# Kernel tuning notes

Hardware: AMD Instinct MI355X
Metric: run time of the kernel (lower is better)

Reference implementation:

```python
import jax, jax.numpy as jnp
import numpy as np

B, S, D, H = 2, 2048, 768, 12
DH = D // H  # 64


def setup_inputs() -> dict:
    key = jax.random.key(0)
    ks = jax.random.split(key, 8)
    std = 1.0 / np.sqrt(D)
    return {
        "q": jax.random.normal(ks[0], (B, S, D), dtype=jnp.float32),
        "k": jax.random.normal(ks[1], (B, S, D), dtype=jnp.float32),
        "v": jax.random.normal(ks[2], (B, S, D), dtype=jnp.float32),
        "Wq": jax.random.normal(ks[3], (D, D), dtype=jnp.float32) * std,
        "bq": jnp.zeros((D,), dtype=jnp.float32),
        "Wk": jax.random.normal(ks[4], (D, D), dtype=jnp.float32) * std,
        "bk": jnp.zeros((D,), dtype=jnp.float32),
        "Wv": jax.random.normal(ks[5], (D, D), dtype=jnp.float32) * std,
        "bv": jnp.zeros((D,), dtype=jnp.float32),
        "Wo": jax.random.normal(ks[6], (D, D), dtype=jnp.float32) * std,
        "bo": jnp.zeros((D,), dtype=jnp.float32),
    }


def reference(q, k, v, Wq, bq, Wk, bk, Wv, bv, Wo, bo):
    b, s, d = q.shape
    # linear projections then split heads: [b, s, d] -> [b, h, s, dh]
    def split(x):
        return x.reshape(b, s, H, DH).transpose(0, 2, 1, 3)

    qh = split(q @ Wq + bq)
    kh = split(k @ Wk + bk)
    vh = split(v @ Wv + bv)

    scale = 1.0 / jnp.sqrt(jnp.asarray(DH, dtype=q.dtype))
    # full [b, h, s, s] score matrix (faithful to the original unfused op)
    scores = jnp.einsum("bhqd,bhkd->bhqk", qh, kh) * scale
    # look-ahead mask: 1 above the diagonal, added as mask * -1e9
    look_ahead = jnp.triu(jnp.ones((s, s), dtype=scores.dtype), k=1)
    scores = scores + look_ahead * (-1e9)

    attn = jax.nn.softmax(scores, axis=-1)  # dropout is identity at inference
    ctx = jnp.einsum("bhqk,bhkd->bhqd", attn, vh)
    ctx = ctx.transpose(0, 2, 1, 3).reshape(b, s, d)
    return ctx @ Wo + bo
```

## Files before the change

kernel.cpp:

```cpp
#include <hip/hip_runtime.h>
#include <hip/hip_bf16.h>
#include <stdint.h>

#define Bz 2
#define Sz 2048
#define Dz 768
#define Hz 12
#define DHz 64
#define Mz (Bz*Sz)
#define NQT16 128

typedef __attribute__((ext_vector_type(4))) float f32x4;
typedef __attribute__((ext_vector_type(8))) short bf16x8;
typedef unsigned short u16;
typedef __attribute__((ext_vector_type(8))) unsigned short u16x8;

__device__ __forceinline__ u16 f2bf(float f) {
  union { float f; uint32_t u; } c; c.f = f;
  uint32_t u = c.u;
  return (u16)((u + 0x7fffu + ((u >> 16) & 1u)) >> 16);
}

__device__ __forceinline__ uint32_t packbf(float lo, float hi) {
  return (uint32_t)f2bf(lo) | ((uint32_t)f2bf(hi) << 16);
}

#define GLL16(gsrc, ldst) \
  __builtin_amdgcn_global_load_lds((const __attribute__((address_space(1))) void*)(gsrc), \
                                   (__attribute__((address_space(3))) void*)(ldst), 16, 0, 0)

__device__ __forceinline__ f32x4 mfma16(bf16x8 a, bf16x8 b, f32x4 c) {
  return __builtin_amdgcn_mfma_f32_16x16x32_bf16(a, b, c, 0, 0, 0);
}

#define CVTB 1536
__global__ __launch_bounds__(256) void prep_kernel(
    const float* __restrict__ qa, const float* __restrict__ ka, const float* __restrict__ va,
    u16* __restrict__ qo, u16* __restrict__ ko, u16* __restrict__ vo,
    const float* __restrict__ W0, const float* __restrict__ W1,
    const float* __restrict__ W2, const float* __restrict__ W3,
    u16* __restrict__ T0, u16* __restrict__ T1,
    u16* __restrict__ T2, u16* __restrict__ T3)
{
  __shared__ float tile[32][33];
  int bid = blockIdx.x;
  if (bid < 3 * CVTB) {
    int z = bid / CVTB;
    int i = (bid % CVTB) * 256 + threadIdx.x;
    const float* src = (z == 0) ? qa : (z == 1) ? ka : va;
    u16* dst = (z == 0) ? qo : (z == 1) ? ko : vo;
    const float4* s4 = (const float4*)src;
    float4 a = s4[(size_t)i * 2];
    float4 b = s4[(size_t)i * 2 + 1];
    u16x8 o;
    o[0] = f2bf(a.x); o[1] = f2bf(a.y); o[2] = f2bf(a.z); o[3] = f2bf(a.w);
    o[4] = f2bf(b.x); o[5] = f2bf(b.y); o[6] = f2bf(b.z); o[7] = f2bf(b.w);
    *(u16x8*)(dst + (size_t)i * 8) = o;
  } else {
    int w = bid - 3 * CVTB;
    int z = w / 576;
    int rem = w - z * 576;
    int by = rem / 24, bxi = rem - by * 24;
    const float* W = (z == 0) ? W0 : (z == 1) ? W1 : (z == 2) ? W2 : W3;
    u16* Wt = (z == 0) ? T0 : (z == 1) ? T1 : (z == 2) ? T2 : T3;
    int bx = bxi * 32, byy = by * 32;
    int tx = threadIdx.x & 31, ty = threadIdx.x >> 5;
#pragma unroll
    for (int i = 0; i < 32; i += 8)
      tile[ty + i][tx] = W[(size_t)(byy + ty + i) * Dz + bx + tx];
    __syncthreads();
#pragma unroll
    for (int i = 0; i < 32; i += 8)
      Wt[(size_t)(bx + ty + i) * Dz + byy + tx] = f2bf(tile[tx][ty + i]);
  }
}

__device__ __forceinline__ void gemm_core(
    const u16* __restrict__ A, const u16* __restrict__ Wt,
    const float* __restrict__ bias, void* __restrict__ out, int mode, float oscale,
    u16 (*As)[128 * 32], u16 (*Bs)[128 * 32])
{
  const int tid = threadIdx.x;
  const int wid = tid >> 6, lane = tid & 63;
  const int wm = wid >> 1, wn = wid & 1;
  const int m0 = blockIdx.x * 128, n0 = blockIdx.y * 128;
  const int fq = lane >> 4, fr = lane & 15;

  int aoff[2];
#pragma unroll
  for (int c = 0; c < 2; ++c) {
    int off  = (wid * 2 + c) * 1024 + lane * 16;
    int row  = off >> 6;
    int colb = (off & 63) ^ (((row >> 1) & 3) << 4);
    aoff[c]  = row * Dz + (colb >> 1);
  }

  int raddr[4], rbaddr[4];
#pragma unroll
  for (int f = 0; f < 4; ++f) {
    int rowA = wm * 64 + f * 16 + fr;
    raddr[f]  = rowA * 64 + ((fq * 16) ^ (((rowA >> 1) & 3) << 4));
    int rowB = wn * 64 + f * 16 + fr;
    rbaddr[f] = rowB * 64 + ((fq * 16) ^ (((rowB >> 1) & 3) << 4));
  }

  f32x4 acc[4][4];
  const f32x4 zero = {0.f, 0.f, 0.f, 0.f};
#pragma unroll
  for (int i = 0; i < 4; ++i)
#pragma unroll
    for (int j = 0; j < 4; ++j) acc[i][j] = zero;

  const u16* Abase = A + (size_t)m0 * Dz;
  const u16* Bbase = Wt + (size_t)n0 * Dz;

  const int NKT = Dz / 32;
#pragma unroll
  for (int c = 0; c < 2; ++c) {
    GLL16(Abase + aoff[c], (char*)As[0] + (wid * 2 + c) * 1024);
    GLL16(Bbase + aoff[c], (char*)Bs[0] + (wid * 2 + c) * 1024);
  }
  int cur = 0;

  for (int kt = 0; kt < NKT; ++kt) {
    int nx = cur + 1; if (nx == 3) nx = 0;
    if (kt + 1 < NKT) {
      int ke = (kt + 1) * 32;
#pragma unroll
      for (int c = 0; c < 2; ++c) {
        GLL16(Abase + ke + aoff[c], (char*)As[nx] + (wid * 2 + c) * 1024);
        GLL16(Bbase + ke + aoff[c], (char*)Bs[nx] + (wid * 2 + c) * 1024);
      }
      asm volatile("s_waitcnt vmcnt(4)" ::: "memory");
    } else {
      asm volatile("s_waitcnt vmcnt(0)" ::: "memory");
    }
    __builtin_amdgcn_s_barrier();
    __builtin_amdgcn_sched_barrier(0);

    bf16x8 af[4], bf[4];
#pragma unroll
    for (int f = 0; f < 4; ++f) {
      af[f] = *(const bf16x8*)((const char*)As[cur] + raddr[f]);
      bf[f] = *(const bf16x8*)((const char*)Bs[cur] + rbaddr[f]);
    }
    __builtin_amdgcn_s_setprio(1);
#pragma unroll
    for (int i = 0; i < 4; ++i)
#pragma unroll
      for (int j = 0; j < 4; ++j)
        acc[i][j] = mfma16(af[i], bf[j], acc[i][j]);
    __builtin_amdgcn_s_setprio(0);
    cur = nx;
  }

  {
    u16* O = (u16*)out;
#pragma unroll
    for (int i = 0; i < 4; ++i) {
      int grow = m0 + wm * 64 + i * 16 + fq * 4;
#pragma unroll
      for (int j = 0; j < 4; ++j) {
        int gcol = n0 + wn * 64 + j * 16 + fr;
        float bv = bias[gcol];
        int h = gcol >> 6, dh = gcol & 63;
#pragma unroll
        for (int r = 0; r < 4; ++r) {
          int t = grow + r;
          int b = t >> 11, s = t & 2047;
          int bh = b * Hz + h;
          u16 val = f2bf((acc[i][j][r] + bv) * oscale);
          size_t idx;
          if (mode == 0) {
            idx = ((((size_t)bh * 128 + (s >> 4)) * 2 + (dh >> 5)) * 64
                   + ((dh >> 3) & 3) * 16 + (s & 15)) * 8 + (dh & 7);
          } else if (mode == 3) {
            idx = (((((size_t)bh * 32 + (s >> 6)) * 4 + ((s >> 4) & 3)) * 2 + (dh >> 5)) * 64
                   + ((dh >> 3) & 3) * 16 + (s & 15)) * 8 + (dh & 7);
          } else {
            int K  = s & 63;
            int pk = ((K & 15) << 2) | (K >> 4);
            idx = (((((size_t)bh * 32 + (s >> 6)) * 4 + (dh >> 4)) * 2 + (pk >> 5)) * 64
                   + ((pk >> 3) & 3) * 16 + (dh & 15)) * 8 + (pk & 7);
          }
          O[idx] = val;
        }
      }
    }
  }
}

__device__ __forceinline__ void gemm_out_core64(
    const u16* __restrict__ A, const u16* __restrict__ Wt,
    const float* __restrict__ bias, float* __restrict__ O,
    u16 (*As)[64 * 32], u16 (*Bs)[128 * 32])
{
  const int tid = threadIdx.x;
  const int wid = tid >> 6, lane = tid & 63;
  const int wm = wid >> 1, wn = wid & 1;
  const int m0 = blockIdx.x * 64, n0 = blockIdx.y * 128;
  const int fq = lane >> 4, fr = lane & 15;

  int aoff;
  {
    int off  = tid * 16;
    int row  = off >> 6;
    int colb = (off & 63) ^ (((row >> 1) & 3) << 4);
    aoff = row * Dz + (colb >> 1);
  }
  int boff[2];
#pragma unroll
  for (int c = 0; c < 2; ++c) {
    int off  = tid * 16 + c * 4096;
    int row  = off >> 6;
    int colb = (off & 63) ^ (((row >> 1) & 3) << 4);
    boff[c] = row * Dz + (colb >> 1);
  }

  int raddr[2], rbaddr[4];
#pragma unroll
  for (int f = 0; f < 2; ++f) {
    int rowA = wm * 32 + f * 16 + fr;
    raddr[f] = rowA * 64 + ((fq * 16) ^ (((rowA >> 1) & 3) << 4));
  }
#pragma unroll
  for (int f = 0; f < 4; ++f) {
    int rowB = wn * 64 + f * 16 + fr;
    rbaddr[f] = rowB * 64 + ((fq * 16) ^ (((rowB >> 1) & 3) << 4));
  }

  f32x4 acc[2][4];
  const f32x4 zero = {0.f, 0.f, 0.f, 0.f};
#pragma unroll
  for (int i = 0; i < 2; ++i)
#pragma unroll
    for (int j = 0; j < 4; ++j) acc[i][j] = zero;

  const u16* Abase = A + (size_t)m0 * Dz;
  const u16* Bbase = Wt + (size_t)n0 * Dz;

  const int NKT = Dz / 32;
  GLL16(Abase + aoff, (char*)As[0] + tid * 16);
#pragma unroll
  for (int c = 0; c < 2; ++c)
    GLL16(Bbase + boff[c], (char*)Bs[0] + tid * 16 + c * 4096);
  int cur = 0;

  for (int kt = 0; kt < NKT; ++kt) {
    int nx = cur + 1; if (nx == 3) nx = 0;
    if (kt + 1 < NKT) {
      int ke = (kt + 1) * 32;
      GLL16(Abase + ke + aoff, (char*)As[nx] + tid * 16);
#pragma unroll
      for (int c = 0; c < 2; ++c)
        GLL16(Bbase + ke + boff[c], (char*)Bs[nx] + tid * 16 + c * 4096);
      asm volatile("s_waitcnt vmcnt(3)" ::: "memory");
    } else {
      asm volatile("s_waitcnt vmcnt(0)" ::: "memory");
    }
    __builtin_amdgcn_s_barrier();
    __builtin_amdgcn_sched_barrier(0);

    bf16x8 af[2], bf[4];
#pragma unroll
    for (int f = 0; f < 2; ++f)
      af[f] = *(const bf16x8*)((const char*)As[cur] + raddr[f]);
#pragma unroll
    for (int f = 0; f < 4; ++f)
      bf[f] = *(const bf16x8*)((const char*)Bs[cur] + rbaddr[f]);
    __builtin_amdgcn_s_setprio(1);
#pragma unroll
    for (int i = 0; i < 2; ++i)
#pragma unroll
      for (int j = 0; j < 4; ++j)
        acc[i][j] = mfma16(af[i], bf[j], acc[i][j]);
    __builtin_amdgcn_s_setprio(0);
    cur = nx;
  }

#pragma unroll
  for (int i = 0; i < 2; ++i) {
    int grow = m0 + wm * 32 + i * 16 + fq * 4;
#pragma unroll
    for (int j = 0; j < 4; ++j) {
      int gcol = n0 + wn * 64 + j * 16 + fr;
      float bv = bias[gcol];
#pragma unroll
      for (int r = 0; r < 4; ++r)
        O[(size_t)(grow + r) * Dz + gcol] = acc[i][j][r] + bv;
    }
  }
}

#define QSCALE 0.1803368801111404f

__global__ __launch_bounds__(256, 3) void gemm_qkv(
    const u16* __restrict__ qb, const u16* __restrict__ kb, const u16* __restrict__ vb,
    const u16* __restrict__ Wqt, const u16* __restrict__ Wkt, const u16* __restrict__ Wvt,
    const float* __restrict__ bq, const float* __restrict__ bk, const float* __restrict__ bv,
    u16* __restrict__ Qf, u16* __restrict__ Kf, u16* __restrict__ Vf)
{
  __shared__ u16 As[3][128 * 32];
  __shared__ u16 Bs[3][128 * 32];
  const u16* A; const u16* W; const float* bias; u16* out; int mode; float osc;
  if (blockIdx.z == 0)      { A = qb; W = Wqt; bias = bq; out = Qf; mode = 0; osc = QSCALE; }
  else if (blockIdx.z == 1) { A = kb; W = Wkt; bias = bk; out = Kf; mode = 3; osc = 1.f; }
  else                      { A = vb; W = Wvt; bias = bv; out = Vf; mode = 1; osc = 1.f; }
  gemm_core(A, W, bias, out, mode, osc, As, Bs);
}

__global__ __launch_bounds__(256, 4) void gemm_out_k(
    const u16* __restrict__ ctx, const u16* __restrict__ Wot,
    const float* __restrict__ bo, float* __restrict__ out)
{
  __shared__ u16 As[3][64 * 32];
  __shared__ u16 Bs[3][128 * 32];
  gemm_out_core64(ctx, Wot, bo, out, As, Bs);
}

__global__ __launch_bounds__(128, 2) void attn_kernel(
    const u16* __restrict__ Qf, const u16* __restrict__ Kf,
    const u16* __restrict__ Vf, u16* __restrict__ ctx)
{
  __shared__ u16 Ps[2][16 * 64];
  __shared__ float o1buf[64 * 16];
  __shared__ float ml1[2][16];
  const int tid = threadIdx.x, wid = tid >> 6, lane = tid & 63;
  const int fq = lane >> 4, fr = lane & 15;
  const int bh = blockIdx.x;
  const int qt = (NQT16 - 1) - blockIdx.y;
  const int b = bh / Hz, h = bh % Hz;
  const int qbase = qt * 16;
  const int nkt = (qbase + 79) >> 6;

  const bf16x8* Qf8 = (const bf16x8*)Qf + (size_t)bh * 128 * 2 * 64;
  const bf16x8* Kf8 = (const bf16x8*)Kf + (size_t)bh * 32 * 8 * 64;
  const bf16x8* Vf8 = (const bf16x8*)Vf + (size_t)bh * 32 * 8 * 64;

  bf16x8 aq[2];
#pragma unroll
  for (int kk = 0; kk < 2; ++kk)
    aq[kk] = Qf8[((size_t)qt * 2 + kk) * 64 + lane];

  const f32x4 zero = {0.f, 0.f, 0.f, 0.f};
  f32x4 o[4];
#pragma unroll
  for (int i = 0; i < 4; ++i) o[i] = zero;
  float m_r[4], l_r[4];
#pragma unroll
  for (int r = 0; r < 4; ++r) { m_r[r] = -1e30f; l_r[r] = 0.f; }

  char* Pw = (char*)Ps[wid];

  if (wid < nkt) {
    bf16x8 kfr[4][2], vfr[4][2];
#pragma unroll
    for (int j = 0; j < 4; ++j)
#pragma unroll
      for (int kk = 0; kk < 2; ++kk)
        kfr[j][kk] = Kf8[((size_t)wid * 8 + j * 2 + kk) * 64 + lane];

    for (int kt = wid; kt < nkt; kt += 2) {
#pragma unroll
      for (int fo = 0; fo < 4; ++fo)
#pragma unroll
        for (int kk = 0; kk < 2; ++kk)
          vfr[fo][kk] = Vf8[((size_t)kt * 8 + fo * 2 + kk) * 64 + lane];

      f32x4 s[4];
#pragma unroll
      for (int j = 0; j < 4; ++j) s[j] = zero;
      __builtin_amdgcn_s_setprio(1);
#pragma unroll
      for (int j = 0; j < 4; ++j)
#pragma unroll
        for (int kk = 0; kk < 2; ++kk)
          s[j] = mfma16(aq[kk], kfr[j][kk], s[j]);
      __builtin_amdgcn_s_setprio(0);

      if (kt + 2 < nkt) {
#pragma unroll
        for (int j = 0; j < 4; ++j)
#pragma unroll
          for (int kk = 0; kk < 2; ++kk)
            kfr[j][kk] = Kf8[((size_t)(kt + 2) * 8 + j * 2 + kk) * 64 + lane];
      }

      if (kt == nkt - 1) {
#pragma unroll
        for (int j = 0; j < 4; ++j) {
          int keyg = kt * 64 + j * 16 + fr;
#pragma unroll
          for (int r = 0; r < 4; ++r)
            if (keyg > qbase + fq * 4 + r) s[j][r] = -1e30f;
        }
      }

      float mt[4];
#pragma unroll
      for (int r = 0; r < 4; ++r) mt[r] = s[0][r];
#pragma unroll
      for (int j = 1; j < 4; ++j)
#pragma unroll
        for (int r = 0; r < 4; ++r) mt[r] = fmaxf(mt[r], s[j][r]);

      int nd = 0;
#pragma unroll
      for (int r = 0; r < 4; ++r) nd |= (mt[r] > m_r[r] + 8.f) ? 1 : 0;
      if (__any(nd)) {
#pragma unroll
        for (int msk = 1; msk < 16; msk <<= 1)
#pragma unroll
          for (int r = 0; r < 4; ++r) mt[r] = fmaxf(mt[r], __shfl_xor(mt[r], msk));
#pragma unroll
        for (int r = 0; r < 4; ++r) {
          float mn = fmaxf(m_r[r], mt[r]);
          float alpha = __builtin_amdgcn_exp2f(m_r[r] - mn);
          m_r[r] = mn;
          l_r[r] *= alpha;
#pragma unroll
          for (int i = 0; i < 4; ++i) o[i][r] *= alpha;
        }
      }

#pragma unroll
      for (int r = 0; r < 4; ++r) {
        float e0 = __builtin_amdgcn_exp2f(s[0][r] - m_r[r]);
        float e1 = __builtin_amdgcn_exp2f(s[1][r] - m_r[r]);
        float e2 = __builtin_amdgcn_exp2f(s[2][r] - m_r[r]);
        float e3 = __builtin_amdgcn_exp2f(s[3][r] - m_r[r]);
        l_r[r] += (e0 + e1) + (e2 + e3);
        uint2 w;
        w.x = packbf(e0, e1);
        w.y = packbf(e2, e3);
        int qr = fq * 4 + r;
        *(uint2*)(Pw + qr * 128 + ((fr * 8) ^ ((qr & 7) << 4))) = w;
      }

      __builtin_amdgcn_s_setprio(1);
#pragma unroll
      for (int kk = 0; kk < 2; ++kk) {
        int cbP = (kk * 64 + fq * 16) ^ ((fr & 7) << 4);
        bf16x8 pa = *(const bf16x8*)(Pw + fr * 128 + cbP);
#pragma unroll
        for (int fo = 0; fo < 4; ++fo)
          o[fo] = mfma16(pa, vfr[fo][kk], o[fo]);
      }
      __builtin_amdgcn_s_setprio(0);
    }
  }

#pragma unroll
  for (int msk = 1; msk < 16; msk <<= 1)
#pragma unroll
    for (int r = 0; r < 4; ++r) l_r[r] += __shfl_xor(l_r[r], msk);

  if (wid == 1) {
#pragma unroll
    for (int fo = 0; fo < 4; ++fo)
#pragma unroll
      for (int r = 0; r < 4; ++r)
        o1buf[lane * 16 + fo * 4 + r] = o[fo][r];
    if (fr == 0) {
#pragma unroll
      for (int r = 0; r < 4; ++r) {
        ml1[0][fq * 4 + r] = m_r[r];
        ml1[1][fq * 4 + r] = l_r[r];
      }
    }
  }
  __syncthreads();

  if (wid == 0) {
    float a0[4], a1[4], li[4];
#pragma unroll
    for (int r = 0; r < 4; ++r) {
      float m1 = ml1[0][fq * 4 + r];
      float l1 = ml1[1][fq * 4 + r];
      float mm = fmaxf(m_r[r], m1);
      a0[r] = __builtin_amdgcn_exp2f(m_r[r] - mm);
      a1[r] = __builtin_amdgcn_exp2f(m1 - mm);
      li[r] = 1.0f / (l_r[r] * a0[r] + l1 * a1[r]);
    }
#pragma unroll
    for (int fo = 0; fo < 4; ++fo) {
      int dh = fo * 16 + fr;
#pragma unroll
      for (int r = 0; r < 4; ++r) {
        float o1 = o1buf[lane * 16 + fo * 4 + r];
        float val = (o[fo][r] * a0[r] + o1 * a1[r]) * li[r];
        int qg = qbase + fq * 4 + r;
        ctx[((size_t)b * Sz + qg) * Dz + h * DHz + dh] = f2bf(val);
      }
    }
  }
}

extern "C" void kernel_launch(void* const* d_in, const int* in_sizes, int n_in,
                              void* d_out, int out_size, void* d_ws, size_t ws_size,
                              hipStream_t stream) {
  const float* q  = (const float*)d_in[0];
  const float* k  = (const float*)d_in[1];
  const float* v  = (const float*)d_in[2];
  const float* Wq = (const float*)d_in[3];
  const float* bq = (const float*)d_in[4];
  const float* Wk = (const float*)d_in[5];
  const float* bk = (const float*)d_in[6];
  const float* Wv = (const float*)d_in[7];
  const float* bv = (const float*)d_in[8];
  const float* Wo = (const float*)d_in[9];
  const float* bo = (const float*)d_in[10];
  float* out = (float*)d_out;

  char* ws = (char*)d_ws;
  size_t off = 0;
  auto alloc = [&](size_t bytes) {
    void* p = ws + off;
    off += (bytes + 255) & ~(size_t)255;
    return p;
  };
  u16* qb  = (u16*)alloc((size_t)Mz * Dz * 2);
  u16* kb  = (u16*)alloc((size_t)Mz * Dz * 2);
  u16* vb  = (u16*)alloc((size_t)Mz * Dz * 2);
  u16* Wqt = (u16*)alloc((size_t)Dz * Dz * 2);
  u16* Wkt = (u16*)alloc((size_t)Dz * Dz * 2);
  u16* Wvt = (u16*)alloc((size_t)Dz * Dz * 2);
  u16* Wot = (u16*)alloc((size_t)Dz * Dz * 2);
  u16* Qf  = (u16*)alloc((size_t)Bz * Hz * Sz * DHz * 2);
  u16* Kf  = (u16*)alloc((size_t)Bz * Hz * Sz * DHz * 2);
  u16* Vf  = (u16*)alloc((size_t)Bz * Hz * Sz * DHz * 2);
  u16* ctx = (u16*)alloc((size_t)Mz * Dz * 2);

  prep_kernel<<<3 * CVTB + 4 * 576, 256, 0, stream>>>(
      q, k, v, qb, kb, vb, Wq, Wk, Wv, Wo, Wqt, Wkt, Wvt, Wot);

  gemm_qkv<<<dim3(Mz / 128, Dz / 128, 3), 256, 0, stream>>>(
      qb, kb, vb, Wqt, Wkt, Wvt, bq, bk, bv, Qf, Kf, Vf);

  attn_kernel<<<dim3(Bz * Hz, NQT16), 128, 0, stream>>>(Qf, Kf, Vf, ctx);

  gemm_out_k<<<dim3(Mz / 64, Dz / 128), 256, 0, stream>>>(ctx, Wot, bo, out);
}
```

Measured before the change: 89.63 us.

## Split attention KV loop across four waves per query tile

Each attention block now runs four waves instead of two. The waves stride over key tiles by four, and the partial max, sum and output of waves 1–3 are merged by wave 0 through shared memory. This shortens the serial KV loop per query tile, which matters most for long causal rows, and raises the number of waves in flight. In exchange, shared memory and merge work grow, and for short query tiles some waves sit idle.

```diff
diff --git a/kernel.cpp b/kernel.cpp
--- a/kernel.cpp
+++ b/kernel.cpp
@@ -318,13 +318,13 @@
   gemm_out_core64(ctx, Wot, bo, out, As, Bs);
 }
 
-__global__ __launch_bounds__(128, 2) void attn_kernel(
+__global__ __launch_bounds__(256, 4) void attn_kernel(
     const u16* __restrict__ Qf, const u16* __restrict__ Kf,
     const u16* __restrict__ Vf, u16* __restrict__ ctx)
 {
-  __shared__ u16 Ps[2][16 * 64];
-  __shared__ float o1buf[64 * 16];
-  __shared__ float ml1[2][16];
+  __shared__ u16 Ps[4][16 * 64];
+  __shared__ float obuf[3][64 * 16];
+  __shared__ float mlb[3][2][16];
   const int tid = threadIdx.x, wid = tid >> 6, lane = tid & 63;
   const int fq = lane >> 4, fr = lane & 15;
   const int bh = blockIdx.x;
@@ -360,7 +360,7 @@
       for (int kk = 0; kk < 2; ++kk)
         kfr[j][kk] = Kf8[((size_t)wid * 8 + j * 2 + kk) * 64 + lane];
 
-    for (int kt = wid; kt < nkt; kt += 2) {
+    for (int kt = wid; kt < nkt; kt += 4) {
 #pragma unroll
       for (int fo = 0; fo < 4; ++fo)
 #pragma unroll
@@ -378,12 +378,12 @@
           s[j] = mfma16(aq[kk], kfr[j][kk], s[j]);
       __builtin_amdgcn_s_setprio(0);
 
-      if (kt + 2 < nkt) {
+      if (kt + 4 < nkt) {
 #pragma unroll
         for (int j = 0; j < 4; ++j)
 #pragma unroll
           for (int kk = 0; kk < 2; ++kk)
-            kfr[j][kk] = Kf8[((size_t)(kt + 2) * 8 + j * 2 + kk) * 64 + lane];
+            kfr[j][kk] = Kf8[((size_t)(kt + 4) * 8 + j * 2 + kk) * 64 + lane];
       }
 
       if (kt == nkt - 1) {
@@ -455,40 +455,54 @@
 #pragma unroll
     for (int r = 0; r < 4; ++r) l_r[r] += __shfl_xor(l_r[r], msk);
 
-  if (wid == 1) {
+  if (wid > 0) {
 #pragma unroll
     for (int fo = 0; fo < 4; ++fo)
 #pragma unroll
       for (int r = 0; r < 4; ++r)
-        o1buf[lane * 16 + fo * 4 + r] = o[fo][r];
+        obuf[wid - 1][lane * 16 + fo * 4 + r] = o[fo][r];
     if (fr == 0) {
 #pragma unroll
       for (int r = 0; r < 4; ++r) {
-        ml1[0][fq * 4 + r] = m_r[r];
-        ml1[1][fq * 4 + r] = l_r[r];
+        mlb[wid - 1][0][fq * 4 + r] = m_r[r];
+        mlb[wid - 1][1][fq * 4 + r] = l_r[r];
       }
     }
   }
   __syncthreads();
 
   if (wid == 0) {
-    float a0[4], a1[4], li[4];
+    float mm[4], lsum[4], a0[4];
 #pragma unroll
     for (int r = 0; r < 4; ++r) {
-      float m1 = ml1[0][fq * 4 + r];
-      float l1 = ml1[1][fq * 4 + r];
-      float mm = fmaxf(m_r[r], m1);
-      a0[r] = __builtin_amdgcn_exp2f(m_r[r] - mm);
-      a1[r] = __builtin_amdgcn_exp2f(m1 - mm);
-      li[r] = 1.0f / (l_r[r] * a0[r] + l1 * a1[r]);
-    }
+      mm[r] = m_r[r];
+#pragma unroll
+      for (int w = 0; w < 3; ++w) mm[r] = fmaxf(mm[r], mlb[w][0][fq * 4 + r]);
+      a0[r] = __builtin_amdgcn_exp2f(m_r[r] - mm[r]);
+      lsum[r] = l_r[r] * a0[r];
+    }
+    float aw[3][4];
+#pragma unroll
+    for (int w = 0; w < 3; ++w)
+#pragma unroll
+      for (int r = 0; r < 4; ++r) {
+        aw[w][r] = __builtin_amdgcn_exp2f(mlb[w][0][fq * 4 + r] - mm[r]);
+        lsum[r] += mlb[w][1][fq * 4 + r] * aw[w][r];
+      }
+    float li[4];
+#pragma unroll
+    for (int r = 0; r < 4; ++r) li[r] = 1.0f / lsum[r];
+
 #pragma unroll
     for (int fo = 0; fo < 4; ++fo) {
       int dh = fo * 16 + fr;
 #pragma unroll
       for (int r = 0; r < 4; ++r) {
-        float o1 = o1buf[lane * 16 + fo * 4 + r];
-        float val = (o[fo][r] * a0[r] + o1 * a1[r]) * li[r];
+        float val = o[fo][r] * a0[r];
+#pragma unroll
+        for (int w = 0; w < 3; ++w)
+          val += obuf[w][lane * 16 + fo * 4 + r] * aw[w][r];
+        val *= li[r];
         int qg = qbase + fq * 4 + r;
         ctx[((size_t)b * Sz + qg) * Dz + h * DHz + dh] = f2bf(val);
       }
@@ -537,7 +551,7 @@
   gemm_qkv<<<dim3(Mz / 128, Dz / 128, 3), 256, 0, stream>>>(
       qb, kb, vb, Wqt, Wkt, Wvt, bq, bk, bv, Qf, Kf, Vf);
 
-  attn_kernel<<<dim3(Bz * Hz, NQT16), 128, 0, stream>>>(Qf, Kf, Vf, ctx);
+  attn_kernel<<<dim3(Bz * Hz, NQT16), 256, 0, stream>>>(Qf, Kf, Vf, ctx);
 
   gemm_out_k<<<dim3(Mz / 64, Dz / 128), 256, 0, stream>>>(ctx, Wot, bo, out);
 }
```

Result: slower. 109.4 us (+22.0%).
